# Kernel tuning notes

Hardware: AMD Instinct MI355X
Metric: run time of the kernel (lower is better)

The kernel has to match this reference:

```python
import jax, jax.numpy as jnp
import numpy as np

B, H1, W1, C = 16, 32, 32, 256
H2, W2, C2 = 16, 16, 512
H3, W3, C3 = 8, 8, 1024
N1, N2, N3 = H1 * W1, H2 * W2, H3 * W3


def resize_bilinear_legacy(x, out_size):
    """Legacy tf.image.resize_images BILINEAR (align_corners=False,
    half_pixel_centers=False): src = dst * in/out. x: [B, H, W]."""
    def lerp_axis(a, in_size, axis):
        src = jnp.arange(out_size, dtype=jnp.float32) * (in_size / out_size)
        lo = jnp.floor(src).astype(jnp.int32)
        hi = jnp.minimum(lo + 1, in_size - 1)
        fr = (src - lo.astype(jnp.float32))
        shape = [1, 1, 1]
        shape[axis] = out_size
        fr = fr.reshape(shape)
        a_lo = jnp.take(a, lo, axis=axis)
        a_hi = jnp.take(a, hi, axis=axis)
        return a_lo * (1.0 - fr) + a_hi * fr

    x = lerp_axis(x, x.shape[1], axis=1)
    x = lerp_axis(x, x.shape[2], axis=2)
    return x


def setup_inputs() -> dict:
    key = jax.random.key(0)
    ks = jax.random.split(key, 10)
    s = lambda c: 1.0 / np.sqrt(c)
    return {
        "f1": jax.random.normal(ks[0], (B, H1, W1, C), jnp.float32),
        "f2": jax.random.normal(ks[1], (B, H2, W2, C2), jnp.float32),
        "f3": jax.random.normal(ks[2], (B, H3, W3, C3), jnp.float32),
        "w1": jax.random.normal(ks[3], (C, C), jnp.float32) * s(C),
        "b1": jnp.zeros((C,), jnp.float32),
        "w2": jax.random.normal(ks[4], (C2, C), jnp.float32) * s(C2),
        "b2": jnp.zeros((C,), jnp.float32),
        "w3": jax.random.normal(ks[5], (C3, C), jnp.float32) * s(C3),
        "b3": jnp.zeros((C,), jnp.float32),
        # Keras 'uniform' init: U(-0.05, 0.05), shape (1,)
        "a1": jax.random.uniform(ks[6], (1,), jnp.float32, -0.05, 0.05),
        "a2": jax.random.uniform(ks[7], (1,), jnp.float32, -0.05, 0.05),
        "a3": jax.random.uniform(ks[8], (1,), jnp.float32, -0.05, 0.05),
    }


def reference(f1, f2, f3, w1, b1, w2, b2, w3, b3, a1, a2, a3):
    # 1x1 conv projections to C channels
    p1 = jnp.einsum("bhwc,cd->bhwd", f1, w1) + b1          # [B,H1,W1,C]
    p2 = jnp.einsum("bhwc,cd->bhwd", f2, w2) + b2          # [B,H2,W2,C]
    p3 = jnp.einsum("bhwc,cd->bhwd", f3, w3) + b3          # [B,H3,W3,C]

    x1 = p1.reshape(B, N1, C)
    x2 = p2.reshape(B, N2, C)
    x3 = p3.reshape(B, N3, C)

    att1 = jnp.einsum("bnc,bmc->bnm", x1, x1)              # [B,N1,N1]
    att2 = jnp.einsum("bnc,bmc->bnm", x2, x2)              # [B,N2,N2]
    att3 = jnp.einsum("bnc,bmc->bnm", x3, x3)              # [B,N3,N3]

    att2 = resize_bilinear_legacy(att2, N1)                # [B,N1,N1]
    att3 = resize_bilinear_legacy(att3, N1)                # [B,N1,N1]

    att = jax.nn.sigmoid(a1[0] * att1 + a2[0] * att2 + a3[0] * att3)

    out = jnp.einsum("bnm,bmc->bnc", att, x1)              # [B,N1,C]
    return p1 + out.reshape(B, H1, W1, C)
```

## Files before the change

kernel.cpp:

```cpp
#include <hip/hip_runtime.h>

typedef unsigned short ushort_t;
typedef short s16x8 __attribute__((ext_vector_type(8)));
typedef float f32x4 __attribute__((ext_vector_type(4)));

#define MFMA16(a, b, c) __builtin_amdgcn_mfma_f32_16x16x32_bf16((a), (b), (c), 0, 0, 0)

#define BATCH 16
#define N1 1024
#define C1 256
#define N2 256
#define N3 64
#define PB3 64
#define PB2 256
#define PB1 256
#define TST 72

static __device__ __forceinline__ ushort_t f2b(float f) {
    unsigned int u = __builtin_bit_cast(unsigned int, f);
    unsigned int r = (u + 0x7fffu + ((u >> 16) & 1u)) >> 16;
    return (ushort_t)r;
}
static __device__ __forceinline__ float b2f(ushort_t b) {
    unsigned int u = ((unsigned int)b) << 16;
    return __builtin_bit_cast(float, u);
}
static __device__ __forceinline__ s16x8 cvt8(const float* p) {
    f32x4 lo = *reinterpret_cast<const f32x4*>(p);
    f32x4 hi = *reinterpret_cast<const f32x4*>(p + 4);
    s16x8 r;
#pragma unroll
    for (int i = 0; i < 4; ++i) {
        r[i]     = (short)f2b(lo[i]);
        r[i + 4] = (short)f2b(hi[i]);
    }
    return r;
}

template <int BK, int NW>
static __device__ __forceinline__ void stage_tile(
    const ushort_t* __restrict__ g, int rowBase, int rowStride, int kOff,
    ushort_t* lds, int w, int l)
{
    constexpr int SEGS = (128 * BK) / 512;
    constexpr int PW   = SEGS / NW;
    constexpr int LPR  = BK / 8;
    constexpr int RPS  = 512 / BK;
#pragma unroll
    for (int c = 0; c < PW; ++c) {
        int seg = w * PW + c;
        int row = seg * RPS + l / LPR;
        int col = (l % LPR) * 8;
        const ushort_t* src = g + (size_t)(rowBase + row) * rowStride + kOff + col;
        __builtin_amdgcn_global_load_lds(
            (const __attribute__((address_space(1))) unsigned int*)src,
            (__attribute__((address_space(3))) unsigned int*)(lds + seg * 512),
            16, 0, 0);
    }
}

__global__ void k_wt(const float* __restrict__ w1, const float* __restrict__ w2,
                     const float* __restrict__ w3,
                     ushort_t* __restrict__ w1t, ushort_t* __restrict__ w2t,
                     ushort_t* __restrict__ w3t) {
    int i = blockIdx.x * 256 + threadIdx.x;
    if (i < 65536) {
        int d = i >> 8, k = i & 255;
        w1t[i] = f2b(w1[k * 256 + d]);
    } else if (i < 65536 + 131072) {
        int j = i - 65536;
        int d = j >> 9, k = j & 511;
        w2t[j] = f2b(w2[k * 256 + d]);
    } else if (i < 65536 + 131072 + 262144) {
        int j = i - 65536 - 131072;
        int d = j >> 10, k = j & 1023;
        w3t[j] = f2b(w3[k * 256 + d]);
    }
}

template <int K>
static __device__ __forceinline__ void proj16(
    const float* __restrict__ A, const ushort_t* __restrict__ wt,
    const float* __restrict__ bias, ushort_t* __restrict__ xb,
    int tile, int w, int lr, int lk)
{
    int rowBase = tile * 16;
    const float* arow = A + (size_t)(rowBase + lr) * K + lk;
    f32x4 acc[4] = {};
#pragma unroll 4
    for (int kk = 0; kk < K; kk += 32) {
        s16x8 af = cvt8(arow + kk);
#pragma unroll
        for (int t = 0; t < 4; ++t) {
            const ushort_t* bp = wt + (size_t)(w * 64 + t * 16 + lr) * K + kk + lk;
            acc[t] = MFMA16(af, *reinterpret_cast<const s16x8*>(bp), acc[t]);
        }
    }
    int r0 = rowBase + (lk >> 3) * 4;
#pragma unroll
    for (int t = 0; t < 4; ++t) {
        int c = w * 64 + t * 16 + lr;
        float bs = bias[c];
#pragma unroll
        for (int j = 0; j < 4; ++j)
            xb[(size_t)(r0 + j) * 256 + c] = f2b(acc[t][j] + bs);
    }
}

__global__ __launch_bounds__(256) void k_proj(
    const float* __restrict__ f1, const float* __restrict__ f2,
    const float* __restrict__ f3,
    const ushort_t* __restrict__ w1t, const ushort_t* __restrict__ w2t,
    const ushort_t* __restrict__ w3t,
    const float* __restrict__ b1, const float* __restrict__ b2,
    const float* __restrict__ b3,
    ushort_t* __restrict__ x1b, ushort_t* __restrict__ x1t,
    ushort_t* __restrict__ x2b, ushort_t* __restrict__ x3b)
{
    __shared__ ushort_t sT[128 * TST];

    int bid = blockIdx.x;
    int w = threadIdx.x >> 6, l = threadIdx.x & 63;
    int lr = l & 15, g = l >> 4, lk = g * 8;

    if (bid < PB3) {
        proj16<1024>(f3, w3t, b3, x3b, bid, w, lr, lk);
    } else if (bid < PB3 + PB2) {
        proj16<512>(f2, w2t, b2, x2b, bid - PB3, w, lr, lk);
    } else {
        int tile = bid - PB3 - PB2;
        int rowBase = tile * 64;
        const float* arow = f1 + (size_t)(rowBase + w * 16 + lr) * 256 + lk;
        f32x4 acc[16] = {};
#pragma unroll 2
        for (int kk = 0; kk < 256; kk += 32) {
            s16x8 af = cvt8(arow + kk);
#pragma unroll
            for (int t = 0; t < 16; ++t) {
                const ushort_t* bp = w1t + (size_t)(t * 16 + lr) * 256 + kk + lk;
                acc[t] = MFMA16(af, *reinterpret_cast<const s16x8*>(bp), acc[t]);
            }
        }
        int rl0 = w * 16 + g * 4;
        int bIdx = rowBase >> 10, mBase = rowBase & 1023;
#pragma unroll
        for (int p = 0; p < 2; ++p) {
            if (p) __syncthreads();
#pragma unroll
            for (int t = 0; t < 8; ++t) {
                int tt = p * 8 + t;
                int c = tt * 16 + lr;
                float bs = b1[c];
#pragma unroll
                for (int j = 0; j < 4; ++j) {
                    float v = acc[tt][j] + bs;
                    ushort_t bits = f2b(v);
                    x1b[(size_t)(rowBase + rl0 + j) * 256 + c] = bits;
                    sT[(c - p * 128) * TST + rl0 + j] = bits;
                }
            }
            __syncthreads();
            int cl = threadIdx.x >> 1, q = threadIdx.x & 1;
            const uint4* src = reinterpret_cast<const uint4*>(&sT[cl * TST + q * 32]);
            uint4* dst = reinterpret_cast<uint4*>(
                &x1t[(((size_t)bIdx * 256 + p * 128 + cl) << 10) + mBase + q * 32]);
            dst[0] = src[0]; dst[1] = src[1]; dst[2] = src[2]; dst[3] = src[3];
        }
    }
}

__global__ __launch_bounds__(256) void k_xxt(
    const ushort_t* __restrict__ x2b, const ushort_t* __restrict__ x3b,
    float* __restrict__ att2, float* __restrict__ att3)
{
    int bid = blockIdx.x;
    const ushort_t* x; float* att; int n, b, bx, by;
    if (bid < 16) { x = x3b; att = att3; n = 64; b = bid; bx = 0; by = 0; }
    else {
        int j = bid - 16;
        x = x2b; att = att2; n = 256;
        b = j >> 4; bx = (j & 15) & 3; by = (j & 15) >> 2;
    }
    int w = threadIdx.x >> 6, l = threadIdx.x & 63;
    int lr = l & 15, lk = (l >> 4) * 8;
    int rowBase = bx * 64 + (w >> 1) * 32;
    int colBase = by * 64 + (w & 1) * 32;
    const ushort_t* xb = x + (size_t)b * n * 256;

    f32x4 acc[2][2] = {};
#pragma unroll 2
    for (int kk = 0; kk < 256; kk += 32) {
        s16x8 a[2], bb[2];
#pragma unroll
        for (int i = 0; i < 2; ++i)
            a[i] = *reinterpret_cast<const s16x8*>(xb + (size_t)(rowBase + i * 16 + lr) * 256 + kk + lk);
#pragma unroll
        for (int j = 0; j < 2; ++j)
            bb[j] = *reinterpret_cast<const s16x8*>(xb + (size_t)(colBase + j * 16 + lr) * 256 + kk + lk);
#pragma unroll
        for (int i = 0; i < 2; ++i)
#pragma unroll
            for (int j = 0; j < 2; ++j)
                acc[i][j] = MFMA16(a[i], bb[j], acc[i][j]);
    }
    float* ab = att + (size_t)b * n * n;
#pragma unroll
    for (int i = 0; i < 2; ++i)
#pragma unroll
        for (int j = 0; j < 2; ++j)
#pragma unroll
            for (int q = 0; q < 4; ++q) {
                int r = rowBase + i * 16 + (l >> 4) * 4 + q;
                int c = colBase + j * 16 + lr;
                ab[(size_t)r * n + c] = acc[i][j][q];
            }
}

__global__ __launch_bounds__(256) void k_att(
    const ushort_t* __restrict__ x1b,
    const float* __restrict__ att2, const float* __restrict__ att3,
    const float* __restrict__ a1p, const float* __restrict__ a2p,
    const float* __restrict__ a3p, ushort_t* __restrict__ att)
{
    __shared__ ushort_t As[2][128 * 32];
    __shared__ ushort_t Bs[2][128 * 32];

    int i = blockIdx.x;
    int b = (i & 7) | ((i >> 9) << 3);
    int tile = (i >> 3) & 63;
    int rowT = (tile >> 3) * 128, colT = (tile & 7) * 128;

    int w = threadIdx.x >> 6, l = threadIdx.x & 63;
    int idx = l & 15, g = l >> 4;
    int rowHalf = w >> 1, colHalf = w & 1;

    const ushort_t* X = x1b + (size_t)b * N1 * C1;

    stage_tile<32, 4>(X, rowT, 256, 0, As[0], w, l);
    stage_tile<32, 4>(X, colT, 256, 0, Bs[0], w, l);

    f32x4 acc[4][4] = {};
    for (int t = 0; t < 8; ++t) {
        __syncthreads();
        if (t < 7) {
            stage_tile<32, 4>(X, rowT, 256, (t + 1) * 32, As[(t + 1) & 1], w, l);
            stage_tile<32, 4>(X, colT, 256, (t + 1) * 32, Bs[(t + 1) & 1], w, l);
        }
        const ushort_t* Ab = As[t & 1];
        const ushort_t* Bb = Bs[t & 1];
        s16x8 af[4], bf[4];
#pragma unroll
        for (int ii = 0; ii < 4; ++ii)
            af[ii] = *reinterpret_cast<const s16x8*>(Ab + (rowHalf * 64 + ii * 16 + idx) * 32 + g * 8);
#pragma unroll
        for (int jj = 0; jj < 4; ++jj)
            bf[jj] = *reinterpret_cast<const s16x8*>(Bb + (colHalf * 64 + jj * 16 + idx) * 32 + g * 8);
#pragma unroll
        for (int ii = 0; ii < 4; ++ii)
#pragma unroll
            for (int jj = 0; jj < 4; ++jj)
                acc[ii][jj] = MFMA16(af[ii], bf[jj], acc[ii][jj]);
    }

    float a1 = *a1p, a2 = *a2p, a3 = *a3p;
    const float* A2 = att2 + (size_t)b * N2 * N2;
    const float* A3 = att3 + (size_t)b * N3 * N3;
    ushort_t* ab = att + (size_t)b * N1 * N1;
    int rowW = rowT + rowHalf * 64, colW = colT + colHalf * 64;

#pragma unroll
    for (int ii = 0; ii < 4; ++ii)
#pragma unroll
        for (int jj = 0; jj < 4; ++jj)
#pragma unroll
            for (int q = 0; q < 4; ++q) {
                int nn = rowW + ii * 16 + g * 4 + q;
                int mm = colW + jj * 16 + idx;
                int r2l = nn >> 2, c2l = mm >> 2;
                int r2h = min(r2l + 1, N2 - 1), c2h = min(c2l + 1, N2 - 1);
                float fr2 = (float)(nn & 3) * 0.25f, fc2 = (float)(mm & 3) * 0.25f;
                float v2 =
                    (1.f - fr2) * ((1.f - fc2) * A2[r2l * N2 + c2l] + fc2 * A2[r2l * N2 + c2h]) +
                    fr2 * ((1.f - fc2) * A2[r2h * N2 + c2l] + fc2 * A2[r2h * N2 + c2h]);
                int r3l = nn >> 4, c3l = mm >> 4;
                int r3h = min(r3l + 1, N3 - 1), c3h = min(c3l + 1, N3 - 1);
                float fr3 = (float)(nn & 15) * 0.0625f, fc3 = (float)(mm & 15) * 0.0625f;
                float v3 =
                    (1.f - fr3) * ((1.f - fc3) * A3[r3l * N3 + c3l] + fc3 * A3[r3l * N3 + c3h]) +
                    fr3 * ((1.f - fc3) * A3[r3h * N3 + c3l] + fc3 * A3[r3h * N3 + c3h]);
                float s = a1 * acc[ii][jj][q] + a2 * v2 + a3 * v3;
                float sig = 1.f / (1.f + __expf(-s));
                ab[(size_t)nn * N1 + mm] = f2b(sig);
            }
}

__global__ __launch_bounds__(512) void k_pv(
    const ushort_t* __restrict__ att, const ushort_t* __restrict__ x1t,
    const ushort_t* __restrict__ x1b, float* __restrict__ out)
{
    __shared__ ushort_t As[2][128 * 64];
    __shared__ ushort_t Bs[2][128 * 64];

    int i = blockIdx.x;
    int b = (i & 7) | (((i >> 7) & 1) << 3);
    int tile = (i >> 3) & 15;
    int rowT = (tile & 7) * 128, colT = (tile >> 3) * 128;

    int w = threadIdx.x >> 6, l = threadIdx.x & 63;
    int idx = l & 15, g = l >> 4;
    int rowHalf = w >> 2;
    int colQ = w & 3;

    const ushort_t* A = att + (size_t)b * N1 * N1;
    const ushort_t* B = x1t + (size_t)b * C1 * N1;

    stage_tile<64, 8>(A, rowT, 1024, 0, As[0], w, l);
    stage_tile<64, 8>(B, colT, 1024, 0, Bs[0], w, l);

    f32x4 acc[4][2] = {};
    for (int t = 0; t < 16; ++t) {
        __syncthreads();
        if (t < 15) {
            stage_tile<64, 8>(A, rowT, 1024, (t + 1) * 64, As[(t + 1) & 1], w, l);
            stage_tile<64, 8>(B, colT, 1024, (t + 1) * 64, Bs[(t + 1) & 1], w, l);
        }
        const ushort_t* Ab = As[t & 1];
        const ushort_t* Bb = Bs[t & 1];
#pragma unroll
        for (int kk = 0; kk < 64; kk += 32) {
            s16x8 af[4], bf[2];
#pragma unroll
            for (int ii = 0; ii < 4; ++ii)
                af[ii] = *reinterpret_cast<const s16x8*>(Ab + (rowHalf * 64 + ii * 16 + idx) * 64 + kk + g * 8);
#pragma unroll
            for (int jj = 0; jj < 2; ++jj)
                bf[jj] = *reinterpret_cast<const s16x8*>(Bb + (colQ * 32 + jj * 16 + idx) * 64 + kk + g * 8);
#pragma unroll
            for (int ii = 0; ii < 4; ++ii)
#pragma unroll
                for (int jj = 0; jj < 2; ++jj)
                    acc[ii][jj] = MFMA16(af[ii], bf[jj], acc[ii][jj]);
        }
    }
    int rowW = rowT + rowHalf * 64, colW = colT + colQ * 32;
#pragma unroll
    for (int ii = 0; ii < 4; ++ii)
#pragma unroll
        for (int jj = 0; jj < 2; ++jj)
#pragma unroll
            for (int q = 0; q < 4; ++q) {
                int r = rowW + ii * 16 + g * 4 + q;
                int c = colW + jj * 16 + idx;
                size_t o = ((size_t)b * N1 + r) * C1 + c;
                out[o] = b2f(x1b[(size_t)b * N1 * C1 + (size_t)r * 256 + c]) + acc[ii][jj][q];
            }
}

extern "C" void kernel_launch(void* const* d_in, const int* in_sizes, int n_in,
                              void* d_out, int out_size, void* d_ws, size_t ws_size,
                              hipStream_t stream) {
    const float* f1 = (const float*)d_in[0];
    const float* f2 = (const float*)d_in[1];
    const float* f3 = (const float*)d_in[2];
    const float* w1 = (const float*)d_in[3];
    const float* b1 = (const float*)d_in[4];
    const float* w2 = (const float*)d_in[5];
    const float* b2 = (const float*)d_in[6];
    const float* w3 = (const float*)d_in[7];
    const float* b3 = (const float*)d_in[8];
    const float* a1 = (const float*)d_in[9];
    const float* a2 = (const float*)d_in[10];
    const float* a3 = (const float*)d_in[11];

    char* ws = (char*)d_ws;
    size_t off = 0;
    auto alloc = [&](size_t bytes) -> void* {
        void* p = ws + off;
        off += (bytes + 255) & ~(size_t)255;
        return p;
    };
    ushort_t* w1t = (ushort_t*)alloc((size_t)256 * 256 * 2);
    ushort_t* w2t = (ushort_t*)alloc((size_t)256 * 512 * 2);
    ushort_t* w3t = (ushort_t*)alloc((size_t)256 * 1024 * 2);
    ushort_t* x1b = (ushort_t*)alloc((size_t)BATCH * N1 * C1 * 2);
    ushort_t* x1t = (ushort_t*)alloc((size_t)BATCH * N1 * C1 * 2);
    ushort_t* x2b = (ushort_t*)alloc((size_t)BATCH * N2 * C1 * 2);
    ushort_t* x3b = (ushort_t*)alloc((size_t)BATCH * N3 * C1 * 2);
    float*    att2 = (float*)alloc((size_t)BATCH * N2 * N2 * 4);
    float*    att3 = (float*)alloc((size_t)BATCH * N3 * N3 * 4);
    ushort_t* attb = (ushort_t*)alloc((size_t)BATCH * N1 * N1 * 2);

    k_wt<<<(65536 + 131072 + 262144 + 255) / 256, 256, 0, stream>>>(w1, w2, w3, w1t, w2t, w3t);

    k_proj<<<PB3 + PB2 + PB1, 256, 0, stream>>>(f1, f2, f3, w1t, w2t, w3t,
                                                b1, b2, b3, x1b, x1t, x2b, x3b);

    k_xxt<<<16 + 256, 256, 0, stream>>>(x2b, x3b, att2, att3);

    k_att<<<1024, 256, 0, stream>>>(x1b, att2, att3, a1, a2, a3, attb);

    k_pv<<<256, 512, 0, stream>>>(attb, x1t, x1b, (float*)d_out);
}
```

Baseline: 213.8 us.

## Tile weight transpose, split-K projections, stage resize patches in LDS

```diff
diff --git a/kernel.cpp b/kernel.cpp
--- a/kernel.cpp
+++ b/kernel.cpp
@@ -11,10 +11,10 @@
 #define C1 256
 #define N2 256
 #define N3 64
-#define PB3 64
-#define PB2 256
-#define PB1 256
-#define TST 72
+#define QB3 64
+#define QB2 256
+#define QB1 1024
+#define PSS 260
 
 static __device__ __forceinline__ ushort_t f2b(float f) {
     unsigned int u = __builtin_bit_cast(unsigned int, f);
@@ -59,51 +59,116 @@
     }
 }
 
-__global__ void k_wt(const float* __restrict__ w1, const float* __restrict__ w2,
-                     const float* __restrict__ w3,
-                     ushort_t* __restrict__ w1t, ushort_t* __restrict__ w2t,
-                     ushort_t* __restrict__ w3t) {
-    int i = blockIdx.x * 256 + threadIdx.x;
-    if (i < 65536) {
-        int d = i >> 8, k = i & 255;
-        w1t[i] = f2b(w1[k * 256 + d]);
-    } else if (i < 65536 + 131072) {
-        int j = i - 65536;
-        int d = j >> 9, k = j & 511;
-        w2t[j] = f2b(w2[k * 256 + d]);
-    } else if (i < 65536 + 131072 + 262144) {
-        int j = i - 65536 - 131072;
-        int d = j >> 10, k = j & 1023;
-        w3t[j] = f2b(w3[k * 256 + d]);
-    }
+__global__ __launch_bounds__(256) void k_wt(
+    const float* __restrict__ w1, const float* __restrict__ w2,
+    const float* __restrict__ w3,
+    ushort_t* __restrict__ w1t, ushort_t* __restrict__ w2t,
+    ushort_t* __restrict__ w3t)
+{
+    __shared__ float sA[64][65];
+
+    int bid = blockIdx.x;
+    const float* w; ushort_t* wt; int K, ktile, dtile;
+    if (bid < 16)      { w = w1; wt = w1t; K = 256;  int j = bid;      ktile = j >> 2; dtile = j & 3; }
+    else if (bid < 48) { w = w2; wt = w2t; K = 512;  int j = bid - 16; ktile = j >> 2; dtile = j & 3; }
+    else               { w = w3; wt = w3t; K = 1024; int j = bid - 48; ktile = j >> 2; dtile = j & 3; }
+    int k0 = ktile * 64, d0 = dtile * 64;
+
+    int jr = threadIdx.x >> 2, ch = (threadIdx.x & 3) * 16;
+    const float* src = w + (size_t)(k0 + jr) * 256 + d0 + ch;
+#pragma unroll
+    for (int i = 0; i < 16; i += 4)
+        *reinterpret_cast<f32x4*>(&sA[jr][ch + i]) = *reinterpret_cast<const f32x4*>(&src[i]);
+    __syncthreads();
+    int jd = threadIdx.x >> 2, kc = (threadIdx.x & 3) * 16;
+    ushort_t ob[16];
+#pragma unroll
+    for (int i = 0; i < 16; ++i) ob[i] = f2b(sA[kc + i][jd]);
+    uint4* dst = reinterpret_cast<uint4*>(&wt[(size_t)(d0 + jd) * K + k0 + kc]);
+    dst[0] = *reinterpret_cast<uint4*>(&ob[0]);
+    dst[1] = *reinterpret_cast<uint4*>(&ob[8]);
 }
 
 template <int K>
-static __device__ __forceinline__ void proj16(
+static __device__ __forceinline__ void projSplitK(
     const float* __restrict__ A, const ushort_t* __restrict__ wt,
     const float* __restrict__ bias, ushort_t* __restrict__ xb,
-    int tile, int w, int lr, int lk)
-{
+    ushort_t* __restrict__ x1t, int tile, int tid,
+    float* __restrict__ ps0, float* __restrict__ ps1)
+{
+    int w = tid >> 6, l = tid & 63;
+    int lr = l & 15, g = l >> 4, lk = g * 8;
     int rowBase = tile * 16;
-    const float* arow = A + (size_t)(rowBase + lr) * K + lk;
-    f32x4 acc[4] = {};
-#pragma unroll 4
-    for (int kk = 0; kk < K; kk += 32) {
+    constexpr int KW = K / 4;
+    int kbeg = w * KW;
+
+    const float* arow = A + (size_t)(rowBase + lr) * K + kbeg + lk;
+    f32x4 acc[16] = {};
+#pragma unroll
+    for (int kk = 0; kk < KW; kk += 32) {
         s16x8 af = cvt8(arow + kk);
 #pragma unroll
-        for (int t = 0; t < 4; ++t) {
-            const ushort_t* bp = wt + (size_t)(w * 64 + t * 16 + lr) * K + kk + lk;
+        for (int t = 0; t < 16; ++t) {
+            const ushort_t* bp = wt + (size_t)(t * 16 + lr) * K + kbeg + kk + lk;
             acc[t] = MFMA16(af, *reinterpret_cast<const s16x8*>(bp), acc[t]);
         }
     }
-    int r0 = rowBase + (lk >> 3) * 4;
-#pragma unroll
-    for (int t = 0; t < 4; ++t) {
-        int c = w * 64 + t * 16 + lr;
+    if (w >= 2) {
+        float* dst = (w == 2) ? ps0 : ps1;
+#pragma unroll
+        for (int t = 0; t < 16; ++t)
+#pragma unroll
+            for (int q = 0; q < 4; ++q)
+                dst[(g * 4 + q) * PSS + t * 16 + lr] = acc[t][q];
+    }
+    __syncthreads();
+    if (w < 2) {
+        float* src = (w == 0) ? ps0 : ps1;
+#pragma unroll
+        for (int t = 0; t < 16; ++t)
+#pragma unroll
+            for (int q = 0; q < 4; ++q)
+                acc[t][q] += src[(g * 4 + q) * PSS + t * 16 + lr];
+    }
+    __syncthreads();
+    if (w == 1) {
+#pragma unroll
+        for (int t = 0; t < 16; ++t)
+#pragma unroll
+            for (int q = 0; q < 4; ++q)
+                ps0[(g * 4 + q) * PSS + t * 16 + lr] = acc[t][q];
+    }
+    __syncthreads();
+    if (w == 0) {
+#pragma unroll
+        for (int t = 0; t < 16; ++t)
+#pragma unroll
+            for (int q = 0; q < 4; ++q)
+                ps0[(g * 4 + q) * PSS + t * 16 + lr] += acc[t][q];
+    }
+    __syncthreads();
+
+    {
+        int j = tid >> 4, c0 = (tid & 15) * 16;
+        ushort_t ob[16];
+#pragma unroll
+        for (int u = 0; u < 16; ++u)
+            ob[u] = f2b(ps0[j * PSS + c0 + u] + bias[c0 + u]);
+        uint4* dst = reinterpret_cast<uint4*>(&xb[(size_t)(rowBase + j) * 256 + c0]);
+        dst[0] = *reinterpret_cast<uint4*>(&ob[0]);
+        dst[1] = *reinterpret_cast<uint4*>(&ob[8]);
+    }
+    if (x1t) {
+        int c = tid;
+        int bI = rowBase >> 10, mBase = rowBase & 1023;
         float bs = bias[c];
-#pragma unroll
-        for (int j = 0; j < 4; ++j)
-            xb[(size_t)(r0 + j) * 256 + c] = f2b(acc[t][j] + bs);
+        ushort_t ob[16];
+#pragma unroll
+        for (int j = 0; j < 16; ++j)
+            ob[j] = f2b(ps0[j * PSS + c] + bs);
+        uint4* dst = reinterpret_cast<uint4*>(&x1t[(((size_t)bI * 256 + c) << 10) + mBase]);
+        dst[0] = *reinterpret_cast<uint4*>(&ob[0]);
+        dst[1] = *reinterpret_cast<uint4*>(&ob[8]);
     }
 }
 
@@ -117,56 +182,15 @@
     ushort_t* __restrict__ x1b, ushort_t* __restrict__ x1t,
     ushort_t* __restrict__ x2b, ushort_t* __restrict__ x3b)
 {
-    __shared__ ushort_t sT[128 * TST];
+    __shared__ float ps[2][16 * PSS];
 
     int bid = blockIdx.x;
-    int w = threadIdx.x >> 6, l = threadIdx.x & 63;
-    int lr = l & 15, g = l >> 4, lk = g * 8;
-
-    if (bid < PB3) {
-        proj16<1024>(f3, w3t, b3, x3b, bid, w, lr, lk);
-    } else if (bid < PB3 + PB2) {
-        proj16<512>(f2, w2t, b2, x2b, bid - PB3, w, lr, lk);
-    } else {
-        int tile = bid - PB3 - PB2;
-        int rowBase = tile * 64;
-        const float* arow = f1 + (size_t)(rowBase + w * 16 + lr) * 256 + lk;
-        f32x4 acc[16] = {};
-#pragma unroll 2
-        for (int kk = 0; kk < 256; kk += 32) {
-            s16x8 af = cvt8(arow + kk);
-#pragma unroll
-            for (int t = 0; t < 16; ++t) {
-                const ushort_t* bp = w1t + (size_t)(t * 16 + lr) * 256 + kk + lk;
-                acc[t] = MFMA16(af, *reinterpret_cast<const s16x8*>(bp), acc[t]);
-            }
-        }
-        int rl0 = w * 16 + g * 4;
-        int bIdx = rowBase >> 10, mBase = rowBase & 1023;
-#pragma unroll
-        for (int p = 0; p < 2; ++p) {
-            if (p) __syncthreads();
-#pragma unroll
-            for (int t = 0; t < 8; ++t) {
-                int tt = p * 8 + t;
-                int c = tt * 16 + lr;
-                float bs = b1[c];
-#pragma unroll
-                for (int j = 0; j < 4; ++j) {
-                    float v = acc[tt][j] + bs;
-                    ushort_t bits = f2b(v);
-                    x1b[(size_t)(rowBase + rl0 + j) * 256 + c] = bits;
-                    sT[(c - p * 128) * TST + rl0 + j] = bits;
-                }
-            }
-            __syncthreads();
-            int cl = threadIdx.x >> 1, q = threadIdx.x & 1;
-            const uint4* src = reinterpret_cast<const uint4*>(&sT[cl * TST + q * 32]);
-            uint4* dst = reinterpret_cast<uint4*>(
-                &x1t[(((size_t)bIdx * 256 + p * 128 + cl) << 10) + mBase + q * 32]);
-            dst[0] = src[0]; dst[1] = src[1]; dst[2] = src[2]; dst[3] = src[3];
-        }
-    }
+    if (bid < QB3)
+        projSplitK<1024>(f3, w3t, b3, x3b, nullptr, bid, threadIdx.x, ps[0], ps[1]);
+    else if (bid < QB3 + QB2)
+        projSplitK<512>(f2, w2t, b2, x2b, nullptr, bid - QB3, threadIdx.x, ps[0], ps[1]);
+    else
+        projSplitK<256>(f1, w1t, b1, x1b, x1t, bid - QB3 - QB2, threadIdx.x, ps[0], ps[1]);
 }
 
 __global__ __launch_bounds__(256) void k_xxt(
@@ -235,6 +259,8 @@
     int rowHalf = w >> 1, colHalf = w & 1;
 
     const ushort_t* X = x1b + (size_t)b * N1 * C1;
+    const float* A2 = att2 + (size_t)b * N2 * N2;
+    const float* A3 = att3 + (size_t)b * N3 * N3;
 
     stage_tile<32, 4>(X, rowT, 256, 0, As[0], w, l);
     stage_tile<32, 4>(X, colT, 256, 0, Bs[0], w, l);
@@ -262,9 +288,22 @@
                 acc[ii][jj] = MFMA16(af[ii], bf[jj], acc[ii][jj]);
     }
 
+    __syncthreads();
+    float* patch2 = reinterpret_cast<float*>(&As[0][0]);
+    float* patch3 = reinterpret_cast<float*>(&Bs[0][0]);
+    int r2b = rowT >> 2, c2b = colT >> 2;
+    for (int id = threadIdx.x; id < 33 * 33; id += 256) {
+        int r = id / 33, c = id - r * 33;
+        patch2[r * 36 + c] = A2[min(r2b + r, N2 - 1) * N2 + min(c2b + c, N2 - 1)];
+    }
+    int r3b = rowT >> 4, c3b = colT >> 4;
+    if (threadIdx.x < 81) {
+        int r = threadIdx.x / 9, c = threadIdx.x - r * 9;
+        patch3[r * 12 + c] = A3[min(r3b + r, N3 - 1) * N3 + min(c3b + c, N3 - 1)];
+    }
+    __syncthreads();
+
     float a1 = *a1p, a2 = *a2p, a3 = *a3p;
-    const float* A2 = att2 + (size_t)b * N2 * N2;
-    const float* A3 = att3 + (size_t)b * N3 * N3;
     ushort_t* ab = att + (size_t)b * N1 * N1;
     int rowW = rowT + rowHalf * 64, colW = colT + colHalf * 64;
 
@@ -276,18 +315,18 @@
             for (int q = 0; q < 4; ++q) {
                 int nn = rowW + ii * 16 + g * 4 + q;
                 int mm = colW + jj * 16 + idx;
-                int r2l = nn >> 2, c2l = mm >> 2;
-                int r2h = min(r2l + 1, N2 - 1), c2h = min(c2l + 1, N2 - 1);
+                int rr = (nn - rowT) >> 2, cc = (mm - colT) >> 2;
                 float fr2 = (float)(nn & 3) * 0.25f, fc2 = (float)(mm & 3) * 0.25f;
-                float v2 =
-                    (1.f - fr2) * ((1.f - fc2) * A2[r2l * N2 + c2l] + fc2 * A2[r2l * N2 + c2h]) +
-                    fr2 * ((1.f - fc2) * A2[r2h * N2 + c2l] + fc2 * A2[r2h * N2 + c2h]);
-                int r3l = nn >> 4, c3l = mm >> 4;
-                int r3h = min(r3l + 1, N3 - 1), c3h = min(c3l + 1, N3 - 1);
+                float p00 = patch2[rr * 36 + cc],       p01 = patch2[rr * 36 + cc + 1];
+                float p10 = patch2[(rr + 1) * 36 + cc], p11 = patch2[(rr + 1) * 36 + cc + 1];
+                float e0 = p00 + fc2 * (p01 - p00), e1 = p10 + fc2 * (p11 - p10);
+                float v2 = e0 + fr2 * (e1 - e0);
+                int r3 = (nn - rowT) >> 4, c3 = (mm - colT) >> 4;
                 float fr3 = (float)(nn & 15) * 0.0625f, fc3 = (float)(mm & 15) * 0.0625f;
-                float v3 =
-                    (1.f - fr3) * ((1.f - fc3) * A3[r3l * N3 + c3l] + fc3 * A3[r3l * N3 + c3h]) +
-                    fr3 * ((1.f - fc3) * A3[r3h * N3 + c3l] + fc3 * A3[r3h * N3 + c3h]);
+                float s00 = patch3[r3 * 12 + c3],       s01 = patch3[r3 * 12 + c3 + 1];
+                float s10 = patch3[(r3 + 1) * 12 + c3], s11 = patch3[(r3 + 1) * 12 + c3 + 1];
+                float f0 = s00 + fc3 * (s01 - s00), f1v = s10 + fc3 * (s11 - s10);
+                float v3 = f0 + fr3 * (f1v - f0);
                 float s = a1 * acc[ii][jj][q] + a2 * v2 + a3 * v3;
                 float sig = 1.f / (1.f + __expf(-s));
                 ab[(size_t)nn * N1 + mm] = f2b(sig);
@@ -390,9 +429,9 @@
     float*    att3 = (float*)alloc((size_t)BATCH * N3 * N3 * 4);
     ushort_t* attb = (ushort_t*)alloc((size_t)BATCH * N1 * N1 * 2);
 
-    k_wt<<<(65536 + 131072 + 262144 + 255) / 256, 256, 0, stream>>>(w1, w2, w3, w1t, w2t, w3t);
-
-    k_proj<<<PB3 + PB2 + PB1, 256, 0, stream>>>(f1, f2, f3, w1t, w2t, w3t,
+    k_wt<<<112, 256, 0, stream>>>(w1, w2, w3, w1t, w2t, w3t);
+
+    k_proj<<<QB3 + QB2 + QB1, 256, 0, stream>>>(f1, f2, f3, w1t, w2t, w3t,
                                                 b1, b2, b3, x1b, x1t, x2b, x3b);
 
     k_xxt<<<16 + 256, 256, 0, stream>>>(x2b, x3b, att2, att3);
```

Result: faster. 204.3 us (-4.5%).
